# Kernel optimization log

Measured on AMD Instinct MI355X. Metric: run time of the kernel, lower is better.

The kernel has to match this reference:

```python
import jax, jax.numpy as jnp
import numpy as np

LN_EPS = 1e-5
C_HID = 16  # c: outer-product channel dim
C_Z = 128


def setup_inputs() -> dict:
    key = jax.random.key(0)
    ks = jax.random.split(key, 4)
    B, N, L, c_m = 1, 128, 512, 256
    c, c_z = C_HID, C_Z
    s_in = 1.0 / np.sqrt(c_m)
    s_out = 1.0 / np.sqrt(c * c)
    return {
        "m": jax.random.normal(ks[0], (B, N, L, c_m), jnp.float32),
        "gamma": jnp.ones((c_m,), jnp.float32),
        "beta": jnp.zeros((c_m,), jnp.float32),
        "Wi": jax.random.normal(ks[1], (c_m, c), jnp.float32) * s_in,
        "bi": jnp.zeros((c,), jnp.float32),
        "Wj": jax.random.normal(ks[2], (c_m, c), jnp.float32) * s_in,
        "bj": jnp.zeros((c,), jnp.float32),
        "Wo": jax.random.normal(ks[3], (c * c, c_z), jnp.float32) * s_out,
        "bo": jnp.zeros((c_z,), jnp.float32),
    }


def reference(m, gamma, beta, Wi, bi, Wj, bj, Wo, bo):
    # LayerNorm over c_m
    mu = jnp.mean(m, axis=-1, keepdims=True)
    var = jnp.mean(jnp.square(m - mu), axis=-1, keepdims=True)
    mn = (m - mu) * jax.lax.rsqrt(var + LN_EPS) * gamma + beta
    # dual projections: (B, N, L, c)
    a = mn @ Wi + bi
    b = mn @ Wj + bj
    # mean over MSA sequences N -> (B, L, c)
    a2 = jnp.mean(a, axis=1)
    b2 = jnp.mean(b, axis=1)
    # outer product + output linear fused:
    # einsum('bic,bjd->bijcd') -> reshape (B,L,L,c*c) -> Linear(c*c -> c_z)
    c = a2.shape[-1]
    Wo3 = Wo.reshape(c, c, -1)  # (c, c, c_z)
    out = jnp.einsum('bic,bjd,cdz->bijz', a2, b2, Wo3) + bo
    return out  # (B, L, L, c_z)
```

## Files before the change

### kernel.cpp

```cpp
#include <hip/hip_runtime.h>


#define LN_EPS 1e-5f

constexpr int N_SEQ = 128;
constexpr int L_DIM = 512;
constexpr int CM    = 256;
constexpr int CH    = 16;
constexpr int CZ    = 128;
constexpr int NPART = 4;

__global__ __launch_bounds__(256) void k1_ln_rowsum(
    const float* __restrict__ m, float* __restrict__ partial)
{
  const int l    = blockIdx.x;
  const int p    = blockIdx.y;
  const int t    = threadIdx.x;
  const int wave = t >> 6;
  const int lane = t & 63;

  float s0 = 0.f, s1 = 0.f, s2 = 0.f, s3 = 0.f;
  for (int r = 0; r < 8; ++r) {
    const int n = p * 32 + wave * 8 + r;
    const float4 v = *((const float4*)(m + ((size_t)n * L_DIM + l) * CM) + lane);
    float sum = v.x + v.y + v.z + v.w;
    float sq  = v.x * v.x + v.y * v.y + v.z * v.z + v.w * v.w;
#pragma unroll
    for (int off = 1; off < 64; off <<= 1) {
      sum += __shfl_xor(sum, off, 64);
      sq  += __shfl_xor(sq,  off, 64);
    }
    const float mu   = sum * (1.0f / CM);
    const float var  = sq * (1.0f / CM) - mu * mu;
    const float rstd = rsqrtf(var + LN_EPS);
    s0 += (v.x - mu) * rstd;
    s1 += (v.y - mu) * rstd;
    s2 += (v.z - mu) * rstd;
    s3 += (v.w - mu) * rstd;
  }

  __shared__ float sacc[4][CM];
  *((float4*)&sacc[wave][4 * lane]) = make_float4(s0, s1, s2, s3);
  __syncthreads();
  const float s = sacc[0][t] + sacc[1][t] + sacc[2][t] + sacc[3][t];
  partial[((size_t)p * L_DIM + l) * CM + t] = s;
}

__global__ __launch_bounds__(256) void k2_proj(
    const float* __restrict__ partial,
    const float* __restrict__ gamma, const float* __restrict__ beta,
    const float* __restrict__ Wi, const float* __restrict__ bi,
    const float* __restrict__ Wj, const float* __restrict__ bj,
    const float* __restrict__ Wo,
    float* __restrict__ a2, float* __restrict__ T)
{
  const int l = blockIdx.x;
  const int t = threadIdx.x;

  __shared__ float s_lds[CM];
  __shared__ float pacc[32][9];
  __shared__ float ab[32];

  float s = 0.f;
  for (int p = 0; p < NPART; ++p)
    s += partial[((size_t)p * L_DIM + l) * CM + t];
  s = gamma[t] * s + (float)N_SEQ * beta[t];
  s_lds[t] = s;
  __syncthreads();

  const int ch  = t >> 3;
  const int sub = t & 7;
  const int c   = ch & 15;
  const float* __restrict__ W = (ch < CH) ? Wi : Wj;
  float acc = 0.f;
  for (int k = 0; k < 32; ++k) {
    const int e = sub * 32 + k;
    acc += s_lds[e] * W[e * CH + c];
  }
  pacc[ch][sub] = acc;
  __syncthreads();

  if (t < 32) {
    float a = 0.f;
    for (int q = 0; q < 8; ++q) a += pacc[t][q];
    a = a * (1.0f / N_SEQ) + ((t < CH) ? bi[t] : bj[t - CH]);
    ab[t] = a;
    if (t < CH) a2[l * CH + t] = a;
  }
  __syncthreads();

  const int z   = t & (CZ - 1);
  const int chi = t >> 7;
  for (int q = 0; q < 8; ++q) {
    const int cc = chi * 8 + q;
    float accT = 0.f;
#pragma unroll
    for (int d = 0; d < CH; ++d)
      accT += ab[CH + d] * Wo[(cc * CH + d) * CZ + z];
    T[((size_t)l * CH + cc) * CZ + z] = accT;
  }
}

__global__ __launch_bounds__(256) void k3_out(
    const float* __restrict__ a2, const float* __restrict__ T,
    const float* __restrict__ bo, float* __restrict__ out)
{
  const int j  = blockIdx.x;
  const int ic = blockIdx.y;
  const int t  = threadIdx.x;

  __shared__ float Ts[CH * CZ];
  __shared__ float As[128 * CH];

  {
    const float4* Tg = (const float4*)(T + (size_t)j * CH * CZ);
    float4* Tl = (float4*)Ts;
    Tl[t]       = Tg[t];
    Tl[t + 256] = Tg[t + 256];
    const float4* Ag = (const float4*)(a2 + (size_t)ic * 128 * CH);
    float4* Al = (float4*)As;
    Al[t]       = Ag[t];
    Al[t + 256] = Ag[t + 256];
  }
  __syncthreads();

  const int z4    = t & 31;
  const int ibase = t >> 5;

  float4 Treg[CH];
#pragma unroll
  for (int c = 0; c < CH; ++c)
    Treg[c] = ((const float4*)(Ts + c * CZ))[z4];
  const float4 bov = ((const float4*)bo)[z4];

#define FMA4(av, tv) { acc.x += (av)*(tv).x; acc.y += (av)*(tv).y; \
                       acc.z += (av)*(tv).z; acc.w += (av)*(tv).w; }
  for (int q = 0; q < 16; ++q) {
    const int il = ibase + 8 * q;
    const float4* arow = (const float4*)(As + il * CH);
    const float4 a0 = arow[0], a1 = arow[1], a2v = arow[2], a3 = arow[3];
    float4 acc = bov;
    FMA4(a0.x, Treg[0]);  FMA4(a0.y, Treg[1]);  FMA4(a0.z, Treg[2]);  FMA4(a0.w, Treg[3]);
    FMA4(a1.x, Treg[4]);  FMA4(a1.y, Treg[5]);  FMA4(a1.z, Treg[6]);  FMA4(a1.w, Treg[7]);
    FMA4(a2v.x, Treg[8]); FMA4(a2v.y, Treg[9]); FMA4(a2v.z, Treg[10]); FMA4(a2v.w, Treg[11]);
    FMA4(a3.x, Treg[12]); FMA4(a3.y, Treg[13]); FMA4(a3.z, Treg[14]); FMA4(a3.w, Treg[15]);
    const int i = ic * 128 + il;
    ((float4*)(out + ((size_t)i * L_DIM + j) * CZ))[z4] = acc;
  }
#undef FMA4
}

extern "C" void kernel_launch(void* const* d_in, const int* in_sizes, int n_in,
                              void* d_out, int out_size, void* d_ws, size_t ws_size,
                              hipStream_t stream) {
  const float* m     = (const float*)d_in[0];
  const float* gamma = (const float*)d_in[1];
  const float* beta  = (const float*)d_in[2];
  const float* Wi    = (const float*)d_in[3];
  const float* bi    = (const float*)d_in[4];
  const float* Wj    = (const float*)d_in[5];
  const float* bj    = (const float*)d_in[6];
  const float* Wo    = (const float*)d_in[7];
  const float* bo    = (const float*)d_in[8];
  float* out = (float*)d_out;

  char* ws = (char*)d_ws;
  float* partial = (float*)ws;
  float* a2      = (float*)(ws + (size_t)NPART * L_DIM * CM * 4);
  float* T       = (float*)(ws + (size_t)NPART * L_DIM * CM * 4
                               + (size_t)L_DIM * CH * 4);

  k1_ln_rowsum<<<dim3(L_DIM, NPART), 256, 0, stream>>>(m, partial);
  k2_proj<<<dim3(L_DIM), 256, 0, stream>>>(partial, gamma, beta,
                                           Wi, bi, Wj, bj, Wo, a2, T);
  k3_out<<<dim3(L_DIM, NPART), 256, 0, stream>>>(a2, T, bo, out);
}
```

Measured before the change: 231.5 us.

## Restructure output kernel tiling, add nontemporal stores, batch LN loads

The output kernel now gives each block 8 j columns and 32 i rows. It loads T straight into registers from global memory and reads a2 rows through the cache, so it no longer stages them in shared memory or needs a barrier. Output writes now use nontemporal stores, which should reduce cache pollution on the 128 MB write stream. The LN kernel issues all eight row loads up front to raise memory-level parallelism, at the cost of more registers.

Measured after the change: 214.4 us. 1.08x faster.

```diff
diff --git a/kernel.cpp b/kernel.cpp
--- a/kernel.cpp
+++ b/kernel.cpp
@@ -10,6 +10,8 @@
 constexpr int CZ    = 128;
 constexpr int NPART = 4;
 
+typedef float floatx4 __attribute__((ext_vector_type(4)));
+
 __global__ __launch_bounds__(256) void k1_ln_rowsum(
     const float* __restrict__ m, float* __restrict__ partial)
 {
@@ -19,12 +21,18 @@
   const int wave = t >> 6;
   const int lane = t & 63;
 
-  float s0 = 0.f, s1 = 0.f, s2 = 0.f, s3 = 0.f;
+  float4 v[8];
+#pragma unroll
   for (int r = 0; r < 8; ++r) {
     const int n = p * 32 + wave * 8 + r;
-    const float4 v = *((const float4*)(m + ((size_t)n * L_DIM + l) * CM) + lane);
-    float sum = v.x + v.y + v.z + v.w;
-    float sq  = v.x * v.x + v.y * v.y + v.z * v.z + v.w * v.w;
+    v[r] = *((const float4*)(m + ((size_t)n * L_DIM + l) * CM) + lane);
+  }
+
+  float s0 = 0.f, s1 = 0.f, s2 = 0.f, s3 = 0.f;
+#pragma unroll
+  for (int r = 0; r < 8; ++r) {
+    float sum = v[r].x + v[r].y + v[r].z + v[r].w;
+    float sq  = v[r].x * v[r].x + v[r].y * v[r].y + v[r].z * v[r].z + v[r].w * v[r].w;
 #pragma unroll
     for (int off = 1; off < 64; off <<= 1) {
       sum += __shfl_xor(sum, off, 64);
@@ -33,10 +41,10 @@
     const float mu   = sum * (1.0f / CM);
     const float var  = sq * (1.0f / CM) - mu * mu;
     const float rstd = rsqrtf(var + LN_EPS);
-    s0 += (v.x - mu) * rstd;
-    s1 += (v.y - mu) * rstd;
-    s2 += (v.z - mu) * rstd;
-    s3 += (v.w - mu) * rstd;
+    s0 += (v[r].x - mu) * rstd;
+    s1 += (v[r].y - mu) * rstd;
+    s2 += (v[r].z - mu) * rstd;
+    s3 += (v[r].w - mu) * rstd;
   }
 
   __shared__ float sacc[4][CM];
@@ -105,47 +113,34 @@
     const float* __restrict__ a2, const float* __restrict__ T,
     const float* __restrict__ bo, float* __restrict__ out)
 {
-  const int j  = blockIdx.x;
-  const int ic = blockIdx.y;
   const int t  = threadIdx.x;
-
-  __shared__ float Ts[CH * CZ];
-  __shared__ float As[128 * CH];
-
-  {
-    const float4* Tg = (const float4*)(T + (size_t)j * CH * CZ);
-    float4* Tl = (float4*)Ts;
-    Tl[t]       = Tg[t];
-    Tl[t + 256] = Tg[t + 256];
-    const float4* Ag = (const float4*)(a2 + (size_t)ic * 128 * CH);
-    float4* Al = (float4*)As;
-    Al[t]       = Ag[t];
-    Al[t + 256] = Ag[t + 256];
-  }
-  __syncthreads();
-
-  const int z4    = t & 31;
-  const int ibase = t >> 5;
+  const int z4 = t & 31;
+  const int j  = blockIdx.x * 8 + (t >> 5);
+  const int i0 = blockIdx.y * 32;
 
   float4 Treg[CH];
+  {
+    const float4* Tg = (const float4*)T + (size_t)j * (CH * 32) + z4;
 #pragma unroll
-  for (int c = 0; c < CH; ++c)
-    Treg[c] = ((const float4*)(Ts + c * CZ))[z4];
+    for (int c = 0; c < CH; ++c)
+      Treg[c] = Tg[c * 32];
+  }
   const float4 bov = ((const float4*)bo)[z4];
 
 #define FMA4(av, tv) { acc.x += (av)*(tv).x; acc.y += (av)*(tv).y; \
                        acc.z += (av)*(tv).z; acc.w += (av)*(tv).w; }
-  for (int q = 0; q < 16; ++q) {
-    const int il = ibase + 8 * q;
-    const float4* arow = (const float4*)(As + il * CH);
-    const float4 a0 = arow[0], a1 = arow[1], a2v = arow[2], a3 = arow[3];
+  for (int ii = 0; ii < 32; ++ii) {
+    const int i = i0 + ii;
+    const float4* ar4 = (const float4*)(a2 + (size_t)i * CH);
+    const float4 a0 = ar4[0], a1 = ar4[1], a2v = ar4[2], a3 = ar4[3];
     float4 acc = bov;
     FMA4(a0.x, Treg[0]);  FMA4(a0.y, Treg[1]);  FMA4(a0.z, Treg[2]);  FMA4(a0.w, Treg[3]);
     FMA4(a1.x, Treg[4]);  FMA4(a1.y, Treg[5]);  FMA4(a1.z, Treg[6]);  FMA4(a1.w, Treg[7]);
     FMA4(a2v.x, Treg[8]); FMA4(a2v.y, Treg[9]); FMA4(a2v.z, Treg[10]); FMA4(a2v.w, Treg[11]);
     FMA4(a3.x, Treg[12]); FMA4(a3.y, Treg[13]); FMA4(a3.z, Treg[14]); FMA4(a3.w, Treg[15]);
-    const int i = ic * 128 + il;
-    ((float4*)(out + ((size_t)i * L_DIM + j) * CZ))[z4] = acc;
+    floatx4* dst = (floatx4*)(out + ((size_t)i * L_DIM + j) * CZ) + z4;
+    floatx4 accv = { acc.x, acc.y, acc.z, acc.w };
+    __builtin_nontemporal_store(accv, dst);
   }
 #undef FMA4
 }
@@ -173,5 +168,5 @@
   k1_ln_rowsum<<<dim3(L_DIM, NPART), 256, 0, stream>>>(m, partial);
   k2_proj<<<dim3(L_DIM), 256, 0, stream>>>(partial, gamma, beta,
                                            Wi, bi, Wj, bj, Wo, a2, T);
-  k3_out<<<dim3(L_DIM, NPART), 256, 0, stream>>>(a2, T, bo, out);
+  k3_out<<<dim3(64, 16), 256, 0, stream>>>(a2, T, bo, out);
 }
```
